# Kernel tuning notes

Measured on AMD Instinct MI355X. Metric: run time of the kernel, lower is better.

Reference implementation:

```python
import jax, jax.numpy as jnp
import numpy as np

B, S, IN_DIM, D, H, L, C = 8, 1024, 256, 1024, 16, 6, 10
DK = D // H
EPS = 1e-5


def setup_inputs() -> dict:
    key = jax.random.key(0)
    ks = iter(jax.random.split(key, 64))
    n = lambda shape, s=0.02: jax.random.normal(next(ks), shape, dtype=jnp.float32) * s
    inp = {
        'x': jax.random.normal(next(ks), (B, S, IN_DIM), dtype=jnp.float32),
        'emb_w': n((IN_DIM, D)), 'emb_b': jnp.zeros((D,), jnp.float32),
        'Wq': n((L, D, D)), 'bq': jnp.zeros((L, D), jnp.float32),
        'Wk': n((L, D, D)), 'bk': jnp.zeros((L, D), jnp.float32),
        'Wv': n((L, D, D)), 'bv': jnp.zeros((L, D), jnp.float32),
        'Wo': n((L, D, D)), 'bo': jnp.zeros((L, D), jnp.float32),
        'W1': n((L, D, 4 * D)), 'b1': jnp.zeros((L, 4 * D), jnp.float32),
        'W2': n((L, 4 * D, D)), 'b2': jnp.zeros((L, D), jnp.float32),
        'ln1_s': jnp.ones((L, D), jnp.float32), 'ln1_b': jnp.zeros((L, D), jnp.float32),
        'ln2_s': jnp.ones((L, D), jnp.float32), 'ln2_b': jnp.zeros((L, D), jnp.float32),
        'fc_w': n((D, C)), 'fc_b': jnp.zeros((C,), jnp.float32),
    }
    return inp


def _pos_encoding_rows(n_rows):
    # Faithful to the torch module: pe is [max_len,1,D]; pe[:x.size(0)] picks the
    # first `batch` positions and broadcasts over the sequence dim.
    pos = jnp.arange(n_rows, dtype=jnp.float32)[:, None]
    div = jnp.exp(jnp.arange(0, D, 2, dtype=jnp.float32) * (-np.log(10000.0) / D))
    pe = jnp.zeros((n_rows, D), jnp.float32)
    pe = pe.at[:, 0::2].set(jnp.sin(pos * div)).at[:, 1::2].set(jnp.cos(pos * div))
    return pe


def _layer_norm(x, scale, bias):
    mu = jnp.mean(x, axis=-1, keepdims=True)
    var = jnp.mean(jnp.square(x - mu), axis=-1, keepdims=True)
    return (x - mu) * jax.lax.rsqrt(var + EPS) * scale + bias


def reference(x, emb_w, emb_b, Wq, bq, Wk, bk, Wv, bv, Wo, bo,
              W1, b1, W2, b2, ln1_s, ln1_b, ln2_s, ln2_b, fc_w, fc_b):
    h = x @ emb_w + emb_b                              # [B,S,D]
    h = h + _pos_encoding_rows(B)[:, None, :]          # broadcast pe[:B] over seq
    scale = 1.0 / np.sqrt(DK)
    for i in range(L):
        def heads(y, W, b):
            return (y @ W + b).reshape(B, S, H, DK).transpose(0, 2, 1, 3)  # bhsd
        q = heads(h, Wq[i], bq[i])
        k = heads(h, Wk[i], bk[i])
        v = heads(h, Wv[i], bv[i])
        scores = jnp.einsum('bhqd,bhkd->bhqk', q, k) * scale
        p = jax.nn.softmax(scores, axis=-1)
        o = jnp.einsum('bhqk,bhkd->bhqd', p, v)
        o = o.transpose(0, 2, 1, 3).reshape(B, S, D)
        attn_out = o @ Wo[i] + bo[i]
        h = _layer_norm(h + attn_out, ln1_s[i], ln1_b[i])
        ff = jax.nn.relu(h @ W1[i] + b1[i]) @ W2[i] + b2[i]
        h = _layer_norm(h + ff, ln2_s[i], ln2_b[i])
    pooled = jnp.mean(h, axis=1)                       # [B,D]
    return pooled @ fc_w + fc_b                        # [B,C]
```

## Files before the change

kernel.cpp:

```cpp
#include <hip/hip_runtime.h>
#include <stdint.h>

#define B_   8
#define S_   1024
#define IND  256
#define D_   1024
#define H_   16
#define DKH  64
#define L_   6
#define FF   4096
#define NTOK (B_*S_)

typedef __bf16 bf16;
typedef __attribute__((ext_vector_type(4))) float  f32x4;
typedef __attribute__((ext_vector_type(8))) __bf16 bf16x8;
typedef __attribute__((ext_vector_type(4))) __bf16 bf16x4;
typedef __attribute__((ext_vector_type(2))) __bf16 bf16x2;

#define AS1 __attribute__((address_space(1)))
#define AS3 __attribute__((address_space(3)))

__device__ __forceinline__ void gload16(const void* g, void* l) {
  __builtin_amdgcn_global_load_lds((AS1 void*)(const_cast<void*>(g)), (AS3 void*)l, 16, 0, 0);
}

__global__ __launch_bounds__(256)
void k_trans(const float* __restrict__ in, bf16* __restrict__ out,
             int K, int N, long inStride, long outStride) {
  __shared__ float t[32][33];
  const float* inp = in + (long)blockIdx.z * inStride;
  bf16* outp = out + (long)blockIdx.z * outStride;
  const int n0 = blockIdx.x * 32, k0 = blockIdx.y * 32;
  const int tx = threadIdx.x & 31, ty = threadIdx.x >> 5;
  #pragma unroll
  for (int j = 0; j < 32; j += 8)
    t[ty + j][tx] = inp[(long)(k0 + ty + j) * N + n0 + tx];
  __syncthreads();
  #pragma unroll
  for (int j = 0; j < 32; j += 8)
    outp[(long)(n0 + ty + j) * K + k0 + tx] = (bf16)t[tx][ty + j];
}

__global__ __launch_bounds__(256)
void k_f2b(const float* __restrict__ in, bf16* __restrict__ out) {
  const long i = ((long)blockIdx.x * 256 + threadIdx.x) * 4;
  f32x4 v = *(const f32x4*)(in + i);
  bf16x4 o;
  #pragma unroll
  for (int j = 0; j < 4; ++j) o[j] = (bf16)v[j];
  *(bf16x4*)(out + i) = o;
}

__global__ __launch_bounds__(256)
void k_pe(float* __restrict__ pe) {
  const int i = blockIdx.x * 256 + threadIdx.x;
  const int b = i >> 10, d = i & 1023;
  const float k2 = (float)(d & ~1);
  const float dv = __expf(k2 * (-9.210340371976184f / (float)D_));
  const float a = (float)b * dv;
  pe[i] = (d & 1) ? cosf(a) : sinf(a);
}

__global__ __launch_bounds__(256)
void k_packb(const float* __restrict__ bq, const float* __restrict__ bk,
             const float* __restrict__ bv, float* __restrict__ out) {
  const int i = blockIdx.x * 256 + threadIdx.x;
  const int l = i / 3072, j = i % 3072;
  const float* src = (j < 1024) ? bq : ((j < 2048) ? bk : bv);
  out[i] = src[l * 1024 + (j & 1023)];
}

template<int EPI>
__global__ __launch_bounds__(256)
void k_gemm(const bf16* __restrict__ A, const bf16* __restrict__ Bt,
            const float* __restrict__ bias,
            void* __restrict__ out0, void* __restrict__ out1,
            const float* __restrict__ pe,
            int M, int N, int K) {
  __shared__ __align__(16) bf16 sA[128 * 32];
  __shared__ __align__(16) bf16 sB[128 * 32];
  const int tid = threadIdx.x;
  const int lane = tid & 63, wv = tid >> 6;
  const int bx = blockIdx.x, by = blockIdx.y;
  const int wm = wv >> 1, wn = wv & 1;
  const int lg = lane >> 4, lc = lane & 15;
  const long arow0 = (long)by * 128;
  const long brow0 = (long)bx * 128;
  const int c0 = (wv * 2 + 0) * 64 + lane;
  const int c1 = (wv * 2 + 1) * 64 + lane;
  const int r0 = c0 >> 2, s0 = c0 & 3;
  const int r1 = c1 >> 2, s1 = c1 & 3;
  bf16* ldsA0 = sA + (wv * 2 + 0) * 512;
  bf16* ldsA1 = sA + (wv * 2 + 1) * 512;
  bf16* ldsB0 = sB + (wv * 2 + 0) * 512;
  bf16* ldsB1 = sB + (wv * 2 + 1) * 512;
  const bf16* Ab = A + arow0 * K;
  const bf16* Bb = Bt + brow0 * K;
  f32x4 acc[4][4] = {};
  const int kT = K >> 5;
  for (int kt = 0; kt < kT; ++kt) {
    const int k0 = kt << 5;
    gload16(Ab + (long)r0 * K + k0 + s0 * 8, ldsA0);
    gload16(Ab + (long)r1 * K + k0 + s1 * 8, ldsA1);
    gload16(Bb + (long)r0 * K + k0 + s0 * 8, ldsB0);
    gload16(Bb + (long)r1 * K + k0 + s1 * 8, ldsB1);
    __syncthreads();
    bf16x8 af[4], bfr[4];
    #pragma unroll
    for (int mr = 0; mr < 4; ++mr)
      af[mr] = *(const bf16x8*)(sA + (wm * 64 + mr * 16 + lc) * 32 + lg * 8);
    #pragma unroll
    for (int nc = 0; nc < 4; ++nc)
      bfr[nc] = *(const bf16x8*)(sB + (wn * 64 + nc * 16 + lc) * 32 + lg * 8);
    #pragma unroll
    for (int mr = 0; mr < 4; ++mr)
      #pragma unroll
      for (int nc = 0; nc < 4; ++nc)
        acc[mr][nc] = __builtin_amdgcn_mfma_f32_16x16x32_bf16(af[mr], bfr[nc], acc[mr][nc], 0, 0, 0);
    __syncthreads();
  }
  #pragma unroll
  for (int mr = 0; mr < 4; ++mr) {
    const int row0 = by * 128 + wm * 64 + mr * 16 + lg * 4;
    #pragma unroll
    for (int nc = 0; nc < 4; ++nc) {
      const int col = bx * 128 + wn * 64 + nc * 16 + lc;
      const float bvv = bias[col];
      #pragma unroll
      for (int r = 0; r < 4; ++r) {
        float v = acc[mr][nc][r] + bvv;
        const long rr = row0 + r;
        if constexpr (EPI == 0) {
          ((bf16*)out0)[rr * N + col] = (bf16)v;
        } else {
          const long bb = rr >> 10;
          v += pe[bb * D_ + col];
          ((float*)out0)[rr * N + col] = v;
          ((bf16*)out1)[rr * N + col] = (bf16)v;
        }
      }
    }
  }
}

template<int EPI>
__global__ __launch_bounds__(512, 2)
void k_gemm256(const bf16* __restrict__ A, const bf16* __restrict__ Bt,
               const float* __restrict__ bias,
               void* __restrict__ out0, void* __restrict__ out1,
               int M, int N, int K) {
  __shared__ __align__(16) bf16 lds[65536];
  const int tid = threadIdx.x;
  const int lane = tid & 63, wv = tid >> 6;
  const int wm = wv >> 2, wn = wv & 3;
  const int lg = lane >> 4, lc = lane & 15;
  const int tileRow = blockIdx.y * 256, tileCol = blockIdx.x * 256;
  const bf16* Abase = A + (long)tileRow * K;
  const bf16* Bbase = Bt + (long)tileCol * K;
  const long laneOff = (long)lc * K + lg * 8;
  f32x4 acc[8][4] = {};
  const int NT = K >> 6;
  const int NI = NT >> 1;

  auto stA = [&](int t, int h, int bb) {
    const int rg = h * 16 + wv * 2;
    const int mb = rg >> 1;
    const bf16* s = Abase + (long)(mb * 16) * K + t * 64 + laneOff;
    bf16* d = lds + bb * 32768 + rg * 512;
    gload16(s, d);
    gload16(s + 32, d + 512);
  };
  auto stB = [&](int t, int h, int bb) {
    const int rg = h * 16 + wv * 2;
    const int mb = rg >> 1;
    const bf16* s = Bbase + (long)(mb * 16) * K + t * 64 + laneOff;
    bf16* d = lds + bb * 32768 + 16384 + rg * 512;
    gload16(s, d);
    gload16(s + 32, d + 512);
  };

  bf16x8 aF[8];
  bf16x8 bF0[4], bF1[4];

#define LDA(BB, MH) do { _Pragma("unroll") for (int m = 0; m < 4; ++m) \
    _Pragma("unroll") for (int kk = 0; kk < 2; ++kk) \
      aF[m*2+kk] = *(const bf16x8*)(lds + (BB)*32768 + ((wm*8 + (MH)*4 + m)*2 + kk)*512 + lane*8); \
  } while(0)
#define LDB(BB, NH, DST) do { _Pragma("unroll") for (int n = 0; n < 2; ++n) \
    _Pragma("unroll") for (int kk = 0; kk < 2; ++kk) \
      DST[n*2+kk] = *(const bf16x8*)(lds + (BB)*32768 + 16384 + ((wn*4 + (NH)*2 + n)*2 + kk)*512 + lane*8); \
  } while(0)
#define MM(MH, NH, BSRC, VM) do { \
    if ((VM) == 1) asm volatile("s_waitcnt vmcnt(4)" ::: "memory"); \
    if ((VM) == 2) asm volatile("s_waitcnt vmcnt(0)" ::: "memory"); \
    __builtin_amdgcn_s_barrier(); \
    __builtin_amdgcn_s_setprio(1); \
    _Pragma("unroll") for (int m = 0; m < 4; ++m) \
      _Pragma("unroll") for (int n = 0; n < 2; ++n) { \
        acc[(MH)*4+m][(NH)*2+n] = __builtin_amdgcn_mfma_f32_16x16x32_bf16(aF[m*2+0], BSRC[n*2+0], acc[(MH)*4+m][(NH)*2+n], 0, 0, 0); \
        acc[(MH)*4+m][(NH)*2+n] = __builtin_amdgcn_mfma_f32_16x16x32_bf16(aF[m*2+1], BSRC[n*2+1], acc[(MH)*4+m][(NH)*2+n], 0, 0, 0); \
      } \
    __builtin_amdgcn_s_setprio(0); \
    __builtin_amdgcn_s_barrier(); \
  } while(0)

  stA(0, 0, 0); stB(0, 0, 0); stA(0, 1, 0); stB(0, 1, 0);
  if (NT > 1) { stA(1, 0, 1); stB(1, 0, 1); }
  asm volatile("s_waitcnt vmcnt(4)" ::: "memory");
  __builtin_amdgcn_s_barrier();

  for (int i = 0; i < NI - 1; ++i) {
    const int t1 = 2 * i + 1, t2 = 2 * i + 2, t3 = 2 * i + 3;
    LDA(0, 0); LDB(0, 0, bF0); stA(t1, 1, 1); MM(0, 0, bF0, 0);
    LDB(0, 1, bF1);            stB(t1, 1, 1); MM(0, 1, bF1, 0);
    LDA(0, 1);                 stA(t2, 0, 0); MM(1, 0, bF0, 0);
                               stB(t2, 0, 0); MM(1, 1, bF1, 1);
    LDA(1, 0); LDB(1, 0, bF0); stA(t2, 1, 0); MM(0, 0, bF0, 0);
    LDB(1, 1, bF1);            stB(t2, 1, 0); MM(0, 1, bF1, 0);
    LDA(1, 1);                 stA(t3, 0, 1); MM(1, 0, bF0, 0);
                               stB(t3, 0, 1); MM(1, 1, bF1, 1);
  }
  {
    const int t1 = NT - 1;
    LDA(0, 0); LDB(0, 0, bF0); stA(t1, 1, 1); MM(0, 0, bF0, 0);
    LDB(0, 1, bF1);            stB(t1, 1, 1); MM(0, 1, bF1, 0);
    LDA(0, 1);                                MM(1, 0, bF0, 0);
                                              MM(1, 1, bF1, 2);
    LDA(1, 0); LDB(1, 0, bF0);                MM(0, 0, bF0, 0);
    LDB(1, 1, bF1);                           MM(0, 1, bF1, 0);
    LDA(1, 1);                                MM(1, 0, bF0, 0);
                                              MM(1, 1, bF1, 0);
  }
#undef LDA
#undef LDB
#undef MM

  #pragma unroll
  for (int mr = 0; mr < 8; ++mr) {
    const int row0 = tileRow + wm * 128 + mr * 16 + lg * 4;
    #pragma unroll
    for (int nr = 0; nr < 4; ++nr) {
      const int col = tileCol + wn * 64 + nr * 16 + lc;
      const float bvv = bias[col];
      if constexpr (EPI == 2) {
        const int which = col >> 10;
        const int hh = (col & 1023) >> 6;
        const int dk = col & 63;
        const long bb = row0 >> 10;
        const int sr = row0 & 1023;
        if (which == 2) {
          bf16x4 pk;
          #pragma unroll
          for (int r = 0; r < 4; ++r) pk[r] = (bf16)(acc[mr][nr][r] + bvv);
          *(bf16x4*)((bf16*)out1 + ((bb * H_ + hh) * (long)DKH + dk) * S_ + sr) = pk;
        } else {
          #pragma unroll
          for (int r = 0; r < 4; ++r) {
            float v = acc[mr][nr][r] + bvv;
            if (which == 0) v *= 0.125f;
            ((bf16*)out0)[(long)which * NTOK * D_ + ((bb * H_ + hh) * (long)S_ + sr + r) * DKH + dk] = (bf16)v;
          }
        }
      } else {
        #pragma unroll
        for (int r = 0; r < 4; ++r) {
          float v = acc[mr][nr][r] + bvv;
          const long rr = row0 + r;
          if constexpr (EPI == 1) v = fmaxf(v, 0.f);
          ((bf16*)out0)[rr * N + col] = (bf16)v;
        }
      }
    }
  }
}

__global__ __launch_bounds__(256)
void k_flash(const bf16* __restrict__ qg, const bf16* __restrict__ kgl,
             const bf16* __restrict__ vtg, bf16* __restrict__ og) {
  __shared__ __align__(16) bf16 sK[64 * 64];
  __shared__ __align__(16) bf16 sV[64 * 64];
  __shared__ __align__(16) bf16 sP[4 * 16 * 64];
  const int tid = threadIdx.x, lane = tid & 63, wv = tid >> 6;
  const int lg = lane >> 4, lc = lane & 15;
  const int bh = blockIdx.y, qt = blockIdx.x;
  const long base = (long)bh * S_ * DKH;
  const bf16* qb = qg + base;
  const bf16* kb = kgl + base;
  const bf16* vb = vtg + base;
  const int qrow = qt * 64 + wv * 16 + lc;
  const bf16x8 qf0 = *(const bf16x8*)(qb + (long)qrow * DKH + lg * 8);
  const bf16x8 qf1 = *(const bf16x8*)(qb + (long)qrow * DKH + 32 + lg * 8);
  float mrun = -3e38f, lrun = 0.f;
  f32x4 oacc[4] = {};
  bf16* sPw = sP + wv * (16 * 64);
  const int swzP = (lc & 7) << 4;
  const int c0 = wv * 128 + lane, c1 = c0 + 64;
  const int r0 = c0 >> 3, sl0 = (c0 & 7) ^ (r0 & 7);
  const int r1 = c1 >> 3, sl1 = (c1 & 7) ^ (r1 & 7);
  bf16* dst0 = sK + c0 * 8 - lane * 8;
  bf16* dst1 = sK + c1 * 8 - lane * 8;
  bf16* dstV0 = sV + c0 * 8 - lane * 8;
  bf16* dstV1 = sV + c1 * 8 - lane * 8;
  for (int kt = 0; kt < S_ / 64; ++kt) {
    const int gk = kt * 64;
    gload16(kb + (long)(gk + r0) * DKH + sl0 * 8, dst0);
    gload16(kb + (long)(gk + r1) * DKH + sl1 * 8, dst1);
    gload16(vb + (long)r0 * S_ + gk + sl0 * 8, dstV0);
    gload16(vb + (long)r1 * S_ + gk + sl1 * 8, dstV1);
    __syncthreads();
    f32x4 sacc[4] = {};
    #pragma unroll
    for (int nc = 0; nc < 4; ++nc) {
      const int kr = nc * 16 + lc;
      bf16x8 k0 = *(const bf16x8*)((char*)sK + kr * 128 + (((0 + lg) ^ (kr & 7)) << 4));
      bf16x8 k1 = *(const bf16x8*)((char*)sK + kr * 128 + (((4 + lg) ^ (kr & 7)) << 4));
      sacc[nc] = __builtin_amdgcn_mfma_f32_16x16x32_bf16(k0, qf0, sacc[nc], 0, 0, 0);
      sacc[nc] = __builtin_amdgcn_mfma_f32_16x16x32_bf16(k1, qf1, sacc[nc], 0, 0, 0);
    }
    float pm = sacc[0][0];
    #pragma unroll
    for (int nc = 0; nc < 4; ++nc)
      #pragma unroll
      for (int r = 0; r < 4; ++r) pm = fmaxf(pm, sacc[nc][r]);
    pm = fmaxf(pm, __shfl_xor(pm, 16));
    pm = fmaxf(pm, __shfl_xor(pm, 32));
    const float mnew = fmaxf(mrun, pm);
    const float fac = __expf(mrun - mnew);
    float ps = 0.f;
    #pragma unroll
    for (int nc = 0; nc < 4; ++nc)
      #pragma unroll
      for (int r = 0; r < 4; ++r) {
        const float p = __expf(sacc[nc][r] - mnew);
        sacc[nc][r] = p;
        ps += p;
      }
    ps += __shfl_xor(ps, 16);
    ps += __shfl_xor(ps, 32);
    lrun = lrun * fac + ps;
    mrun = mnew;
    #pragma unroll
    for (int nc = 0; nc < 4; ++nc)
      #pragma unroll
      for (int rp = 0; rp < 2; ++rp) {
        bf16x2 t;
        t[0] = (bf16)sacc[nc][rp * 2 + 0];
        t[1] = (bf16)sacc[nc][rp * 2 + 1];
        *(bf16x2*)((char*)sPw + lc * 128 + ((nc * 32 + lg * 8 + rp * 4) ^ swzP)) = t;
      }
    asm volatile("s_waitcnt lgkmcnt(0)" ::: "memory");
    __builtin_amdgcn_sched_barrier(0);
    float fr[4];
    #pragma unroll
    for (int r = 0; r < 4; ++r) fr[r] = __shfl(fac, lg * 4 + r);
    #pragma unroll
    for (int nc = 0; nc < 4; ++nc)
      #pragma unroll
      for (int r = 0; r < 4; ++r) oacc[nc][r] *= fr[r];
    #pragma unroll
    for (int m = 0; m < 2; ++m) {
      const bf16x8 pf = *(const bf16x8*)((char*)sPw + lc * 128 + ((m * 64 + lg * 16) ^ swzP));
      #pragma unroll
      for (int nc = 0; nc < 4; ++nc) {
        const int vr = nc * 16 + lc;
        bf16x8 vf = *(const bf16x8*)((char*)sV + vr * 128 + (((m * 4 + lg) ^ (vr & 7)) << 4));
        oacc[nc] = __builtin_amdgcn_mfma_f32_16x16x32_bf16(pf, vf, oacc[nc], 0, 0, 0);
      }
    }
    __syncthreads();
  }
  const int b = bh >> 4, h = bh & 15;
  const float linv = 1.f / lrun;
  #pragma unroll
  for (int r = 0; r < 4; ++r) {
    const float inv = __shfl(linv, lg * 4 + r);
    const int s = qt * 64 + wv * 16 + lg * 4 + r;
    const long obase = (((long)b * S_ + s) * H_ + h) * DKH;
    #pragma unroll
    for (int nc = 0; nc < 4; ++nc)
      og[obase + nc * 16 + lc] = (bf16)(oacc[nc][r] * inv);
  }
}

__global__ __launch_bounds__(256)
void k_addln(const float* __restrict__ hin, const bf16* __restrict__ dlt,
             const float* __restrict__ sc, const float* __restrict__ bi,
             float* __restrict__ hout, bf16* __restrict__ hbout) {
  const int row = blockIdx.x, t = threadIdx.x;
  const long off = (long)row * D_ + t * 4;
  f32x4 hv = *(const f32x4*)(hin + off);
  bf16x4 dv = *(const bf16x4*)(dlt + off);
  f32x4 x;
  float s = 0.f, ss = 0.f;
  #pragma unroll
  for (int j = 0; j < 4; ++j) { x[j] = hv[j] + (float)dv[j]; s += x[j]; ss += x[j] * x[j]; }
  #pragma unroll
  for (int m = 1; m < 64; m <<= 1) { s += __shfl_xor(s, m); ss += __shfl_xor(ss, m); }
  __shared__ float red[8];
  const int w = t >> 6, ln = t & 63;
  if (ln == 0) { red[w] = s; red[4 + w] = ss; }
  __syncthreads();
  s = red[0] + red[1] + red[2] + red[3];
  ss = red[4] + red[5] + red[6] + red[7];
  const float mu = s * (1.f / D_);
  const float rstd = rsqrtf(ss * (1.f / D_) - mu * mu + 1e-5f);
  f32x4 scv = *(const f32x4*)(sc + t * 4);
  f32x4 biv = *(const f32x4*)(bi + t * 4);
  f32x4 y; bf16x4 yb;
  #pragma unroll
  for (int j = 0; j < 4; ++j) { y[j] = (x[j] - mu) * rstd * scv[j] + biv[j]; yb[j] = (bf16)y[j]; }
  *(f32x4*)(hout + off) = y;
  *(bf16x4*)(hbout + off) = yb;
}

__global__ __launch_bounds__(256)
void k_pool1(const float* __restrict__ h, float* __restrict__ part) {
  const int i = blockIdx.x * 256 + threadIdx.x;
  const int b = i >> 10, d = i & 1023;
  const int s0 = blockIdx.y * 128;
  float s = 0.f;
  for (int t = 0; t < 128; ++t) s += h[((long)b * S_ + s0 + t) * D_ + d];
  part[(long)blockIdx.y * NTOK + i] = s;
}

__global__ __launch_bounds__(256)
void k_pool2(const float* __restrict__ part, float* __restrict__ pooled) {
  const int i = blockIdx.x * 256 + threadIdx.x;
  float s = 0.f;
  #pragma unroll
  for (int j = 0; j < 8; ++j) s += part[(long)j * NTOK + i];
  pooled[i] = s * (1.f / S_);
}

__global__ __launch_bounds__(64)
void k_fc(const float* __restrict__ pooled, const float* __restrict__ fw,
          const float* __restrict__ fb, float* __restrict__ out) {
  const int b = blockIdx.x / 10, c = blockIdx.x % 10;
  const int lane = threadIdx.x;
  float s = 0.f;
  for (int d = lane; d < D_; d += 64) s += pooled[b * D_ + d] * fw[d * 10 + c];
  #pragma unroll
  for (int m = 1; m < 64; m <<= 1) s += __shfl_xor(s, m);
  if (lane == 0) out[b * 10 + c] = s + fb[c];
}

extern "C" void kernel_launch(void* const* d_in, const int* in_sizes, int n_in,
                              void* d_out, int out_size, void* d_ws, size_t ws_size,
                              hipStream_t stream) {
  const float* x     = (const float*)d_in[0];
  const float* emb_w = (const float*)d_in[1];
  const float* emb_b = (const float*)d_in[2];
  const float* Wq    = (const float*)d_in[3];
  const float* bq    = (const float*)d_in[4];
  const float* Wk    = (const float*)d_in[5];
  const float* bk    = (const float*)d_in[6];
  const float* Wv    = (const float*)d_in[7];
  const float* bv    = (const float*)d_in[8];
  const float* Wo    = (const float*)d_in[9];
  const float* bo    = (const float*)d_in[10];
  const float* W1    = (const float*)d_in[11];
  const float* b1    = (const float*)d_in[12];
  const float* W2    = (const float*)d_in[13];
  const float* b2    = (const float*)d_in[14];
  const float* ln1s  = (const float*)d_in[15];
  const float* ln1b  = (const float*)d_in[16];
  const float* ln2s  = (const float*)d_in[17];
  const float* ln2b  = (const float*)d_in[18];
  const float* fcw   = (const float*)d_in[19];
  const float* fcb   = (const float*)d_in[20];

  char* w = (char*)d_ws;
  size_t off = 0;
  auto alloc = [&](size_t bytes) -> char* {
    char* p = w + off;
    off += (bytes + 255) & ~(size_t)255;
    return p;
  };
  bf16*  x_bf  = (bf16*) alloc((size_t)NTOK * IND * 2);
  bf16*  embT  = (bf16*) alloc((size_t)D_ * IND * 2);
  bf16*  qkvT  = (bf16*) alloc((size_t)L_ * 3 * D_ * D_ * 2);
  bf16*  woT   = (bf16*) alloc((size_t)L_ * D_ * D_ * 2);
  bf16*  w1T   = (bf16*) alloc((size_t)L_ * FF * D_ * 2);
  bf16*  w2T   = (bf16*) alloc((size_t)L_ * D_ * FF * 2);
  float* qkvB  = (float*)alloc((size_t)L_ * 3 * D_ * 4);
  float* pe    = (float*)alloc((size_t)B_ * D_ * 4);
  float* h_f   = (float*)alloc((size_t)NTOK * D_ * 4);
  bf16*  h_b   = (bf16*) alloc((size_t)NTOK * D_ * 2);
  bf16*  delta = (bf16*) alloc((size_t)NTOK * D_ * 2);
  float* pooled= (float*)alloc((size_t)B_ * D_ * 4);
  float* part  = (float*)alloc((size_t)8 * NTOK * 4);
  bf16*  scratch = (bf16*)alloc((size_t)NTOK * FF * 2);
  bf16* qb  = scratch;
  bf16* kb  = scratch + (size_t)NTOK * D_;
  bf16* vTb = scratch + (size_t)2 * NTOK * D_;
  bf16* ob  = scratch + (size_t)3 * NTOK * D_;
  bf16* ffn1 = scratch;
  (void)ws_size; (void)in_sizes; (void)n_in; (void)out_size;

  k_f2b<<<dim3(NTOK * IND / 1024), dim3(256), 0, stream>>>(x, x_bf);
  k_trans<<<dim3(D_ / 32, IND / 32, 1), dim3(256), 0, stream>>>(emb_w, embT, IND, D_, 0, 0);
  k_trans<<<dim3(32, 32, L_), dim3(256), 0, stream>>>(Wq, qkvT,               D_, D_, (long)D_ * D_, (long)3 * D_ * D_);
  k_trans<<<dim3(32, 32, L_), dim3(256), 0, stream>>>(Wk, qkvT + D_ * D_,     D_, D_, (long)D_ * D_, (long)3 * D_ * D_);
  k_trans<<<dim3(32, 32, L_), dim3(256), 0, stream>>>(Wv, qkvT + 2 * D_ * D_, D_, D_, (long)D_ * D_, (long)3 * D_ * D_);
  k_trans<<<dim3(32, 32, L_), dim3(256), 0, stream>>>(Wo, woT, D_, D_, (long)D_ * D_, (long)D_ * D_);
  k_trans<<<dim3(FF / 32, 32, L_), dim3(256), 0, stream>>>(W1, w1T, D_, FF, (long)D_ * FF, (long)FF * D_);
  k_trans<<<dim3(32, FF / 32, L_), dim3(256), 0, stream>>>(W2, w2T, FF, D_, (long)FF * D_, (long)D_ * FF);
  k_pe<<<dim3(B_ * D_ / 256), dim3(256), 0, stream>>>(pe);
  k_packb<<<dim3(L_ * 3 * D_ / 256), dim3(256), 0, stream>>>(bq, bk, bv, qkvB);

  k_gemm<3><<<dim3(D_ / 128, NTOK / 128), dim3(256), 0, stream>>>(
      x_bf, embT, emb_b, h_f, h_b, pe, NTOK, D_, IND);

  for (int l = 0; l < L_; ++l) {
    k_gemm256<2><<<dim3(3 * D_ / 256, NTOK / 256), dim3(512), 0, stream>>>(
        h_b, qkvT + (size_t)l * 3 * D_ * D_, qkvB + l * 3 * D_,
        qb, vTb, NTOK, 3 * D_, D_);
    k_flash<<<dim3(S_ / 64, B_ * H_), dim3(256), 0, stream>>>(qb, kb, vTb, ob);
    k_gemm256<0><<<dim3(D_ / 256, NTOK / 256), dim3(512), 0, stream>>>(
        ob, woT + (size_t)l * D_ * D_, bo + l * D_,
        delta, nullptr, NTOK, D_, D_);
    k_addln<<<dim3(NTOK), dim3(256), 0, stream>>>(h_f, delta, ln1s + l * D_, ln1b + l * D_, h_f, h_b);
    k_gemm256<1><<<dim3(FF / 256, NTOK / 256), dim3(512), 0, stream>>>(
        h_b, w1T + (size_t)l * FF * D_, b1 + l * FF,
        ffn1, nullptr, NTOK, FF, D_);
    k_gemm256<0><<<dim3(D_ / 256, NTOK / 256), dim3(512), 0, stream>>>(
        ffn1, w2T + (size_t)l * D_ * FF, b2 + l * D_,
        delta, nullptr, NTOK, D_, FF);
    k_addln<<<dim3(NTOK), dim3(256), 0, stream>>>(h_f, delta, ln2s + l * D_, ln2b + l * D_, h_f, h_b);
  }

  k_pool1<<<dim3(NTOK / 256, 8), dim3(256), 0, stream>>>(h_f, part);
  k_pool2<<<dim3(NTOK / 256), dim3(256), 0, stream>>>(part, pooled);
  k_fc<<<dim3(B_ * 10), dim3(64), 0, stream>>>(pooled, fcw, fcb, (float*)d_out);
}
```

Baseline: 2.656 ms.

## Split-K the N=1024 projection GEMMs and fold partial sums into add-LayerNorm

```diff
diff --git a/kernel.cpp b/kernel.cpp
--- a/kernel.cpp
+++ b/kernel.cpp
@@ -143,11 +143,12 @@
   }
 }
 
-template<int EPI>
+template<int EPI, int SPLIT>
 __global__ __launch_bounds__(512, 2)
 void k_gemm256(const bf16* __restrict__ A, const bf16* __restrict__ Bt,
                const float* __restrict__ bias,
                void* __restrict__ out0, void* __restrict__ out1,
+               float* __restrict__ pout,
                int M, int N, int K) {
   __shared__ __align__(16) bf16 lds[65536];
   const int tid = threadIdx.x;
@@ -155,11 +156,13 @@
   const int wm = wv >> 2, wn = wv & 3;
   const int lg = lane >> 4, lc = lane & 15;
   const int tileRow = blockIdx.y * 256, tileCol = blockIdx.x * 256;
-  const bf16* Abase = A + (long)tileRow * K;
-  const bf16* Bbase = Bt + (long)tileCol * K;
+  const int kHalf = SPLIT ? (K >> 1) : K;
+  const long kOff = SPLIT ? (long)blockIdx.z * kHalf : 0;
+  const bf16* Abase = A + (long)tileRow * K + kOff;
+  const bf16* Bbase = Bt + (long)tileCol * K + kOff;
   const long laneOff = (long)lc * K + lg * 8;
   f32x4 acc[8][4] = {};
-  const int NT = K >> 6;
+  const int NT = kHalf >> 6;
   const int NI = NT >> 1;
 
   auto stA = [&](int t, int h, int bb) {
@@ -191,7 +194,7 @@
       DST[n*2+kk] = *(const bf16x8*)(lds + (BB)*32768 + 16384 + ((wn*4 + (NH)*2 + n)*2 + kk)*512 + lane*8); \
   } while(0)
 #define MM(MH, NH, BSRC, VM) do { \
-    if ((VM) == 1) asm volatile("s_waitcnt vmcnt(4)" ::: "memory"); \
+    if ((VM) == 1) asm volatile("s_waitcnt vmcnt(8)" ::: "memory"); \
     if ((VM) == 2) asm volatile("s_waitcnt vmcnt(0)" ::: "memory"); \
     __builtin_amdgcn_s_barrier(); \
     __builtin_amdgcn_s_setprio(1); \
@@ -205,36 +208,36 @@
   } while(0)
 
   stA(0, 0, 0); stB(0, 0, 0); stA(0, 1, 0); stB(0, 1, 0);
-  if (NT > 1) { stA(1, 0, 1); stB(1, 0, 1); }
-  asm volatile("s_waitcnt vmcnt(4)" ::: "memory");
+  stA(1, 0, 1); stB(1, 0, 1); stA(1, 1, 1); stB(1, 1, 1);
+  asm volatile("s_waitcnt vmcnt(8)" ::: "memory");
   __builtin_amdgcn_s_barrier();
 
   for (int i = 0; i < NI - 1; ++i) {
-    const int t1 = 2 * i + 1, t2 = 2 * i + 2, t3 = 2 * i + 3;
-    LDA(0, 0); LDB(0, 0, bF0); stA(t1, 1, 1); MM(0, 0, bF0, 0);
-    LDB(0, 1, bF1);            stB(t1, 1, 1); MM(0, 1, bF1, 0);
-    LDA(0, 1);                 stA(t2, 0, 0); MM(1, 0, bF0, 0);
-                               stB(t2, 0, 0); MM(1, 1, bF1, 1);
-    LDA(1, 0); LDB(1, 0, bF0); stA(t2, 1, 0); MM(0, 0, bF0, 0);
-    LDB(1, 1, bF1);            stB(t2, 1, 0); MM(0, 1, bF1, 0);
-    LDA(1, 1);                 stA(t3, 0, 1); MM(1, 0, bF0, 0);
-                               stB(t3, 0, 1); MM(1, 1, bF1, 1);
+    const int t2 = 2 * i + 2, t3 = 2 * i + 3;
+    LDA(0, 0); LDB(0, 0, bF0);                    MM(0, 0, bF0, 0);
+    LDB(0, 1, bF1);            stA(t2, 0, 0);     MM(0, 1, bF1, 0);
+    LDA(0, 1);                 stB(t2, 0, 0);     MM(1, 0, bF0, 0);
+                  stA(t2, 1, 0); stB(t2, 1, 0);   MM(1, 1, bF1, 1);
+    LDA(1, 0); LDB(1, 0, bF0);                    MM(0, 0, bF0, 0);
+    LDB(1, 1, bF1);            stA(t3, 0, 1);     MM(0, 1, bF1, 0);
+    LDA(1, 1);                 stB(t3, 0, 1);     MM(1, 0, bF0, 0);
+                  stA(t3, 1, 1); stB(t3, 1, 1);   MM(1, 1, bF1, 1);
   }
   {
-    const int t1 = NT - 1;
-    LDA(0, 0); LDB(0, 0, bF0); stA(t1, 1, 1); MM(0, 0, bF0, 0);
-    LDB(0, 1, bF1);            stB(t1, 1, 1); MM(0, 1, bF1, 0);
-    LDA(0, 1);                                MM(1, 0, bF0, 0);
-                                              MM(1, 1, bF1, 2);
-    LDA(1, 0); LDB(1, 0, bF0);                MM(0, 0, bF0, 0);
-    LDB(1, 1, bF1);                           MM(0, 1, bF1, 0);
-    LDA(1, 1);                                MM(1, 0, bF0, 0);
-                                              MM(1, 1, bF1, 0);
+    LDA(0, 0); LDB(0, 0, bF0);                    MM(0, 0, bF0, 0);
+    LDB(0, 1, bF1);                               MM(0, 1, bF1, 0);
+    LDA(0, 1);                                    MM(1, 0, bF0, 0);
+                                                  MM(1, 1, bF1, 2);
+    LDA(1, 0); LDB(1, 0, bF0);                    MM(0, 0, bF0, 0);
+    LDB(1, 1, bF1);                               MM(0, 1, bF1, 0);
+    LDA(1, 1);                                    MM(1, 0, bF0, 0);
+                                                  MM(1, 1, bF1, 0);
   }
 #undef LDA
 #undef LDB
 #undef MM
 
+  const bool wpart = SPLIT && (blockIdx.z == 1);
   #pragma unroll
   for (int mr = 0; mr < 8; ++mr) {
     const int row0 = tileRow + wm * 128 + mr * 16 + lg * 4;
@@ -242,7 +245,11 @@
     for (int nr = 0; nr < 4; ++nr) {
       const int col = tileCol + wn * 64 + nr * 16 + lc;
       const float bvv = bias[col];
-      if constexpr (EPI == 2) {
+      if (wpart) {
+        #pragma unroll
+        for (int r = 0; r < 4; ++r)
+          pout[(long)(row0 + r) * N + col] = acc[mr][nr][r];
+      } else if constexpr (EPI == 2) {
         const int which = col >> 10;
         const int hh = (col & 1023) >> 6;
         const int dk = col & 63;
@@ -382,18 +389,26 @@
   }
 }
 
+template<int TWO>
 __global__ __launch_bounds__(256)
 void k_addln(const float* __restrict__ hin, const bf16* __restrict__ dlt,
+             const float* __restrict__ p1,
              const float* __restrict__ sc, const float* __restrict__ bi,
              float* __restrict__ hout, bf16* __restrict__ hbout) {
   const int row = blockIdx.x, t = threadIdx.x;
   const long off = (long)row * D_ + t * 4;
   f32x4 hv = *(const f32x4*)(hin + off);
   bf16x4 dv = *(const bf16x4*)(dlt + off);
+  f32x4 pv;
+  if constexpr (TWO) pv = *(const f32x4*)(p1 + off);
   f32x4 x;
   float s = 0.f, ss = 0.f;
   #pragma unroll
-  for (int j = 0; j < 4; ++j) { x[j] = hv[j] + (float)dv[j]; s += x[j]; ss += x[j] * x[j]; }
+  for (int j = 0; j < 4; ++j) {
+    x[j] = hv[j] + (float)dv[j];
+    if constexpr (TWO) x[j] += pv[j];
+    s += x[j]; ss += x[j] * x[j];
+  }
   #pragma unroll
   for (int m = 1; m < 64; m <<= 1) { s += __shfl_xor(s, m); ss += __shfl_xor(ss, m); }
   __shared__ float red[8];
@@ -495,7 +510,9 @@
   bf16* vTb = scratch + (size_t)2 * NTOK * D_;
   bf16* ob  = scratch + (size_t)3 * NTOK * D_;
   bf16* ffn1 = scratch;
-  (void)ws_size; (void)in_sizes; (void)n_in; (void)out_size;
+  float* p1 = (float*)alloc((size_t)NTOK * D_ * 4);
+  const bool canSplit = (off <= ws_size);
+  (void)in_sizes; (void)n_in; (void)out_size;
 
   k_f2b<<<dim3(NTOK * IND / 1024), dim3(256), 0, stream>>>(x, x_bf);
   k_trans<<<dim3(D_ / 32, IND / 32, 1), dim3(256), 0, stream>>>(emb_w, embT, IND, D_, 0, 0);
@@ -512,21 +529,35 @@
       x_bf, embT, emb_b, h_f, h_b, pe, NTOK, D_, IND);
 
   for (int l = 0; l < L_; ++l) {
-    k_gemm256<2><<<dim3(3 * D_ / 256, NTOK / 256), dim3(512), 0, stream>>>(
+    k_gemm256<2, 0><<<dim3(3 * D_ / 256, NTOK / 256), dim3(512), 0, stream>>>(
         h_b, qkvT + (size_t)l * 3 * D_ * D_, qkvB + l * 3 * D_,
-        qb, vTb, NTOK, 3 * D_, D_);
+        qb, vTb, nullptr, NTOK, 3 * D_, D_);
     k_flash<<<dim3(S_ / 64, B_ * H_), dim3(256), 0, stream>>>(qb, kb, vTb, ob);
-    k_gemm256<0><<<dim3(D_ / 256, NTOK / 256), dim3(512), 0, stream>>>(
-        ob, woT + (size_t)l * D_ * D_, bo + l * D_,
-        delta, nullptr, NTOK, D_, D_);
-    k_addln<<<dim3(NTOK), dim3(256), 0, stream>>>(h_f, delta, ln1s + l * D_, ln1b + l * D_, h_f, h_b);
-    k_gemm256<1><<<dim3(FF / 256, NTOK / 256), dim3(512), 0, stream>>>(
+    if (canSplit) {
+      k_gemm256<0, 1><<<dim3(D_ / 256, NTOK / 256, 2), dim3(512), 0, stream>>>(
+          ob, woT + (size_t)l * D_ * D_, bo + l * D_,
+          delta, nullptr, p1, NTOK, D_, D_);
+      k_addln<1><<<dim3(NTOK), dim3(256), 0, stream>>>(h_f, delta, p1, ln1s + l * D_, ln1b + l * D_, h_f, h_b);
+    } else {
+      k_gemm256<0, 0><<<dim3(D_ / 256, NTOK / 256), dim3(512), 0, stream>>>(
+          ob, woT + (size_t)l * D_ * D_, bo + l * D_,
+          delta, nullptr, nullptr, NTOK, D_, D_);
+      k_addln<0><<<dim3(NTOK), dim3(256), 0, stream>>>(h_f, delta, nullptr, ln1s + l * D_, ln1b + l * D_, h_f, h_b);
+    }
+    k_gemm256<1, 0><<<dim3(FF / 256, NTOK / 256), dim3(512), 0, stream>>>(
         h_b, w1T + (size_t)l * FF * D_, b1 + l * FF,
-        ffn1, nullptr, NTOK, FF, D_);
-    k_gemm256<0><<<dim3(D_ / 256, NTOK / 256), dim3(512), 0, stream>>>(
-        ffn1, w2T + (size_t)l * D_ * FF, b2 + l * D_,
-        delta, nullptr, NTOK, D_, FF);
-    k_addln<<<dim3(NTOK), dim3(256), 0, stream>>>(h_f, delta, ln2s + l * D_, ln2b + l * D_, h_f, h_b);
+        ffn1, nullptr, nullptr, NTOK, FF, D_);
+    if (canSplit) {
+      k_gemm256<0, 1><<<dim3(D_ / 256, NTOK / 256, 2), dim3(512), 0, stream>>>(
+          ffn1, w2T + (size_t)l * D_ * FF, b2 + l * D_,
+          delta, nullptr, p1, NTOK, D_, FF);
+      k_addln<1><<<dim3(NTOK), dim3(256), 0, stream>>>(h_f, delta, p1, ln2s + l * D_, ln2b + l * D_, h_f, h_b);
+    } else {
+      k_gemm256<0, 0><<<dim3(D_ / 256, NTOK / 256), dim3(512), 0, stream>>>(
+          ffn1, w2T + (size_t)l * D_ * FF, b2 + l * D_,
+          delta, nullptr, nullptr, NTOK, D_, FF);
+      k_addln<0><<<dim3(NTOK), dim3(256), 0, stream>>>(h_f, delta, nullptr, ln2s + l * D_, ln2b + l * D_, h_f, h_b);
+    }
   }
 
   k_pool1<<<dim3(NTOK / 256, 8), dim3(256), 0, stream>>>(h_f, part);
```

After: 2.389 ms. 10.1% less time.
